# Kernel optimization log

Hardware: AMD Instinct MI355X
Metric: run time of the kernel (lower is better)

Reference implementation:

```python
import jax, jax.numpy as jnp
import numpy as np

THR = 1.0   # snntorch Leaky default threshold
BETA = 0.9  # leak factor from the module


@jax.custom_vjp
def atan_spike(x):
    # Heaviside forward; ATan surrogate gradient (snntorch default alpha=2):
    # d/dx = 1 / (1 + (pi * x)^2)
    return (x > 0).astype(x.dtype)

def _atan_fwd(x):
    return (x > 0).astype(x.dtype), x

def _atan_bwd(x, g):
    return (g / (1.0 + (jnp.pi * x) ** 2),)

atan_spike.defvjp(_atan_fwd, _atan_bwd)


def setup_inputs() -> dict:
    key = jax.random.key(0)
    k0, k1, k2, k3, k4 = jax.random.split(key, 5)
    B, T, L = 256, 1000, 30  # 24 = L - 7 + 1 matches fc1 in_features 16*24
    out_c = 35
    x = jax.random.normal(k0, (B, T, L), dtype=jnp.float32)
    conv_w = jax.random.normal(k1, (16, 1, 7), dtype=jnp.float32) / np.float32(np.sqrt(7.0))
    conv_b = jax.random.normal(k2, (16,), dtype=jnp.float32) * 0.05
    fc_w = jax.random.normal(k3, (out_c, 16 * 24), dtype=jnp.float32) / np.float32(np.sqrt(384.0))
    fc_b = jax.random.normal(k4, (out_c,), dtype=jnp.float32) * 0.05
    return {"x": x, "conv_w": conv_w, "conv_b": conv_b, "fc_w": fc_w, "fc_b": fc_b}


def reference(x, conv_w, conv_b, fc_w, fc_b):
    B, T, L = x.shape
    # Conv1d has no recurrence -> hoist it out of the time loop, batched over B*T.
    cur1 = jax.lax.conv_general_dilated(
        x.reshape(B * T, 1, L), conv_w, window_strides=(1,), padding="VALID",
        dimension_numbers=("NCH", "OIH", "NCH"),
    ) + conv_b[None, :, None]                      # (B*T, 16, 24)
    Lo = cur1.shape[-1]
    cur1 = cur1.reshape(B, T, 16, Lo).transpose(1, 0, 2, 3)  # (T, B, 16, 24)
    out_c = fc_w.shape[0]

    def step(carry, c1):
        mem1, mem2 = carry
        # LIF1: reset-by-subtraction using detached spike of previous membrane
        r1 = jax.lax.stop_gradient((mem1 > THR).astype(mem1.dtype))
        mem1 = BETA * mem1 + c1 - r1 * THR
        spk1 = atan_spike(mem1 - THR)              # (B, 16, 24)
        c2 = spk1.reshape(B, 16 * Lo) @ fc_w.T + fc_b  # (B, out_c)
        # LIF2
        r2 = jax.lax.stop_gradient((mem2 > THR).astype(mem2.dtype))
        mem2 = BETA * mem2 + c2 - r2 * THR
        return (mem1, mem2), mem2

    init = (jnp.zeros((B, 16, Lo), x.dtype), jnp.zeros((B, out_c), x.dtype))
    _, mem2_rec = jax.lax.scan(step, init, cur1)   # (T, B, out_c)
    return mem2_rec.mean(axis=0)                   # (B, out_c)
```

## Files before the change

kernel.cpp:

```cpp
#include <hip/hip_runtime.h>

typedef _Float16 half8 __attribute__((ext_vector_type(8)));
typedef float f32x4 __attribute__((ext_vector_type(4)));

#define SPH  32
#define NIT  34
#define SPKW 392
#define XTW  36
#define C2W  48
#define TN   1000

__global__ __launch_bounds__(768, 1) void snn_fwd(
    const float* __restrict__ x,
    const float* __restrict__ conv_w,
    const float* __restrict__ conv_b,
    const float* __restrict__ fc_w,
    const float* __restrict__ fc_b,
    float* __restrict__ out)
{
    __shared__ __align__(16) _Float16 spk[2][SPH][SPKW];
    __shared__ __align__(16) float    xsT[2][30][XTW];
    __shared__ __align__(16) float    c2L[2][SPH][C2W];

    const int tid  = threadIdx.x;
    const int b    = blockIdx.x;
    const int wid  = tid >> 6;
    const int lane = tid & 63;

    const int ct = tid;
    const int c  = ct / 24;
    const int p  = ct % 24;
    float wk[7];
    float cb = 0.f;
    if (wid < 6) {
#pragma unroll
        for (int k = 0; k < 7; ++k) wk[k] = conv_w[c * 7 + k];
        cb = conv_b[c];
    }

    const int g  = wid - 6;
    const int m  = g >> 1;
    const int tb = g & 1;
    const int nL = lane & 15;
    const int q  = lane >> 4;
    half8 A[12];
    if (wid >= 6) {
        const int o = m * 16 + nL;
#pragma unroll
        for (int kt = 0; kt < 12; ++kt) {
            half8 a;
#pragma unroll
            for (int j = 0; j < 8; ++j) {
                int K = kt * 32 + q * 8 + j;
                a[j] = (o < 35) ? (_Float16)fc_w[o * 384 + K] : (_Float16)0.f;
            }
            A[kt] = a;
        }
    }
    const float fcb = (wid == 6 && lane < 35) ? fc_b[lane] : 0.f;
    const int st = tid - 384;

    float m1 = 0.f, sp = 0.f;
    float mem2 = 0.f, accO = 0.f;

    const float* xb = x + (size_t)b * (TN * 30);

    if (wid >= 6) {
#pragma unroll
        for (int r = 0; r < 3; ++r) {
            int f = st + 384 * r;
            if (f < 960) xsT[0][f % 30][f / 30] = xb[f];
        }
    }
    __syncthreads();

#pragma unroll 1
    for (int ph = 0; ph < NIT; ++ph) {
        if (wid < 6) {
            if (ph < 32) {
                const float* xcol = &xsT[ph & 1][p][0];
                unsigned short* sdst = (unsigned short*)&spk[ph & 1][0][ct];
#pragma unroll 2
                for (int s0 = 0; s0 < SPH; s0 += 4) {
                    f32x4 xv[7];
#pragma unroll
                    for (int k = 0; k < 7; ++k)
                        xv[k] = *(const f32x4*)(xcol + k * XTW + s0);
                    float cc[4];
#pragma unroll
                    for (int dt = 0; dt < 4; ++dt) cc[dt] = cb;
#pragma unroll
                    for (int k = 0; k < 7; ++k) {
#pragma unroll
                        for (int dt = 0; dt < 4; ++dt)
                            cc[dt] = fmaf(wk[k], xv[k][dt], cc[dt]);
                    }
#pragma unroll
                    for (int dt = 0; dt < 4; ++dt) {
                        m1 = fmaf(0.9f, m1, cc[dt] - sp);
                        sp = (m1 > 1.0f) ? 1.0f : 0.0f;
                        sdst[(s0 + dt) * SPKW] =
                            (m1 > 1.0f) ? (unsigned short)0x3C00u : (unsigned short)0u;
                    }
                }
            }
        } else {
            float xr[3];
            const bool stg = (ph <= 30);
            if (stg) {
                const float* src = xb + (ph + 1) * (SPH * 30);
#pragma unroll
                for (int r = 0; r < 3; ++r) {
                    int f = st + 384 * r;
                    int t = (ph + 1) * SPH + f / 30;
                    xr[r] = (f < 960 && t < TN) ? src[f] : 0.f;
                }
            }
            const bool doScan = (wid == 6 && lane < 35 && ph >= 2);
            float v[SPH];
            if (doScan) {
                const float* cs = &c2L[(ph - 2) & 1][0][0];
#pragma unroll
                for (int j = 0; j < SPH; ++j) v[j] = cs[j * C2W + lane];
            }
            if (ph >= 1 && ph <= 32) {
                const _Float16* sb = &spk[(ph - 1) & 1][0][0];
                half8 B[12];
#pragma unroll
                for (int kt = 0; kt < 12; ++kt)
                    B[kt] = *(const half8*)(sb + (tb * 16 + nL) * SPKW + kt * 32 + q * 8);
                f32x4 acc = {0.f, 0.f, 0.f, 0.f};
#pragma unroll
                for (int kt = 0; kt < 12; ++kt)
                    acc = __builtin_amdgcn_mfma_f32_16x16x32_f16(A[kt], B[kt], acc, 0, 0, 0);
                float* cd = &c2L[(ph - 1) & 1][0][0];
                *(f32x4*)(cd + (tb * 16 + nL) * C2W + m * 16 + q * 4) = acc;
            }
            if (doScan) {
                const int tbase = (ph - 2) * SPH;
#pragma unroll
                for (int j = 0; j < SPH; ++j) {
                    float r2 = (mem2 > 1.0f) ? 1.0f : 0.0f;
                    mem2 = 0.9f * mem2 + (v[j] + fcb) - r2;
                    if (tbase + j < TN) accO += mem2;
                }
            }
            if (stg) {
                float* dst = &xsT[(ph + 1) & 1][0][0];
#pragma unroll
                for (int r = 0; r < 3; ++r) {
                    int f = st + 384 * r;
                    if (f < 960) dst[(f % 30) * XTW + (f / 30)] = xr[r];
                }
            }
        }
        __syncthreads();
    }

    if (wid == 6 && lane < 35) out[b * 35 + lane] = accO * (1.0f / (float)TN);
}

extern "C" void kernel_launch(void* const* d_in, const int* in_sizes, int n_in,
                              void* d_out, int out_size, void* d_ws, size_t ws_size,
                              hipStream_t stream) {
    const float* x      = (const float*)d_in[0];
    const float* conv_w = (const float*)d_in[1];
    const float* conv_b = (const float*)d_in[2];
    const float* fc_w   = (const float*)d_in[3];
    const float* fc_b   = (const float*)d_in[4];
    float* out          = (float*)d_out;

    snn_fwd<<<256, 768, 0, stream>>>(x, conv_w, conv_b, fc_w, fc_b, out);
}
```

Measured before the change: 149.9 us.

## Add dedicated staging/scan wavefronts and prefetch input two phases ahead

Grows the block from 12 to 16 wavefronts, so MFMA waves do only the fc matmul and four new waves handle x staging and the LIF2 scan. The global load for x is issued one phase earlier and held in registers across the barrier, which hides global memory latency. The transpose indices are precomputed once. The cost is more threads per block and a changed launch bound, which could affect register allocation.

After: 147.0 us. 1.02x faster.

```diff
diff --git a/kernel.cpp b/kernel.cpp
--- a/kernel.cpp
+++ b/kernel.cpp
@@ -10,7 +10,7 @@
 #define C2W  48
 #define TN   1000
 
-__global__ __launch_bounds__(768, 1) void snn_fwd(
+__global__ __launch_bounds__(1024, 4) void snn_fwd(
     const float* __restrict__ x,
     const float* __restrict__ conv_w,
     const float* __restrict__ conv_b,
@@ -44,7 +44,7 @@
     const int nL = lane & 15;
     const int q  = lane >> 4;
     half8 A[12];
-    if (wid >= 6) {
+    if (wid >= 6 && wid < 12) {
         const int o = m * 16 + nL;
 #pragma unroll
         for (int kt = 0; kt < 12; ++kt) {
@@ -57,19 +57,35 @@
             A[kt] = a;
         }
     }
-    const float fcb = (wid == 6 && lane < 35) ? fc_b[lane] : 0.f;
-    const int st = tid - 384;
+
+    const int st4 = tid - 768;
+    int fs[4], fl[4];
+    if (wid >= 12) {
+#pragma unroll
+        for (int r = 0; r < 4; ++r) {
+            int f = st4 + 256 * r;
+            fs[r] = f / 30;
+            fl[r] = f % 30;
+        }
+    }
+    const float fcb = (wid == 12 && lane < 35) ? fc_b[lane] : 0.f;
 
     float m1 = 0.f, sp = 0.f;
     float mem2 = 0.f, accO = 0.f;
+    float xr[4];
 
     const float* xb = x + (size_t)b * (TN * 30);
 
-    if (wid >= 6) {
+    if (wid >= 12) {
 #pragma unroll
-        for (int r = 0; r < 3; ++r) {
-            int f = st + 384 * r;
-            if (f < 960) xsT[0][f % 30][f / 30] = xb[f];
+        for (int r = 0; r < 4; ++r) {
+            int f = st4 + 256 * r;
+            if (f < 960) xsT[0][fl[r]][fs[r]] = xb[f];
+        }
+#pragma unroll
+        for (int r = 0; r < 4; ++r) {
+            int f = st4 + 256 * r;
+            xr[r] = (f < 960) ? xb[960 + f] : 0.f;
         }
     }
     __syncthreads();
@@ -104,25 +120,7 @@
                     }
                 }
             }
-        } else {
-            float xr[3];
-            const bool stg = (ph <= 30);
-            if (stg) {
-                const float* src = xb + (ph + 1) * (SPH * 30);
-#pragma unroll
-                for (int r = 0; r < 3; ++r) {
-                    int f = st + 384 * r;
-                    int t = (ph + 1) * SPH + f / 30;
-                    xr[r] = (f < 960 && t < TN) ? src[f] : 0.f;
-                }
-            }
-            const bool doScan = (wid == 6 && lane < 35 && ph >= 2);
-            float v[SPH];
-            if (doScan) {
-                const float* cs = &c2L[(ph - 2) & 1][0][0];
-#pragma unroll
-                for (int j = 0; j < SPH; ++j) v[j] = cs[j * C2W + lane];
-            }
+        } else if (wid < 12) {
             if (ph >= 1 && ph <= 32) {
                 const _Float16* sb = &spk[(ph - 1) & 1][0][0];
                 half8 B[12];
@@ -136,7 +134,29 @@
                 float* cd = &c2L[(ph - 1) & 1][0][0];
                 *(f32x4*)(cd + (tb * 16 + nL) * C2W + m * 16 + q * 4) = acc;
             }
-            if (doScan) {
+        } else {
+            if (ph <= 30) {
+                float* dst = &xsT[(ph + 1) & 1][0][0];
+#pragma unroll
+                for (int r = 0; r < 4; ++r) {
+                    int f = st4 + 256 * r;
+                    if (f < 960) dst[fl[r] * XTW + fs[r]] = xr[r];
+                }
+            }
+            if (ph <= 29) {
+                const float* src = xb + (size_t)(ph + 2) * (SPH * 30);
+#pragma unroll
+                for (int r = 0; r < 4; ++r) {
+                    int f = st4 + 256 * r;
+                    int t = (ph + 2) * SPH + fs[r];
+                    xr[r] = (f < 960 && t < TN) ? src[f] : 0.f;
+                }
+            }
+            if (wid == 12 && lane < 35 && ph >= 2) {
+                const float* cs = &c2L[(ph - 2) & 1][0][0];
+                float v[SPH];
+#pragma unroll
+                for (int j = 0; j < SPH; ++j) v[j] = cs[j * C2W + lane];
                 const int tbase = (ph - 2) * SPH;
 #pragma unroll
                 for (int j = 0; j < SPH; ++j) {
@@ -145,19 +165,11 @@
                     if (tbase + j < TN) accO += mem2;
                 }
             }
-            if (stg) {
-                float* dst = &xsT[(ph + 1) & 1][0][0];
-#pragma unroll
-                for (int r = 0; r < 3; ++r) {
-                    int f = st + 384 * r;
-                    if (f < 960) dst[(f % 30) * XTW + (f / 30)] = xr[r];
-                }
-            }
         }
         __syncthreads();
     }
 
-    if (wid == 6 && lane < 35) out[b * 35 + lane] = accO * (1.0f / (float)TN);
+    if (wid == 12 && lane < 35) out[b * 35 + lane] = accO * (1.0f / (float)TN);
 }
 
 extern "C" void kernel_launch(void* const* d_in, const int* in_sizes, int n_in,
@@ -170,5 +182,5 @@
     const float* fc_b   = (const float*)d_in[4];
     float* out          = (float*)d_out;
 
-    snn_fwd<<<256, 768, 0, stream>>>(x, conv_w, conv_b, fc_w, fc_b, out);
+    snn_fwd<<<256, 1024, 0, stream>>>(x, conv_w, conv_b, fc_w, fc_b, out);
 }
```

## Load conv inputs directly from global with register prefetch, drop LDS staging

Applied to the files above, without the earlier changes.

The conv threads now read their 7-tap input windows straight from global memory with unaligned vector loads, prefetching the next four timesteps into registers instead of having MFMA waves stage a transposed x tile in LDS. The conv thread mapping becomes channel-fastest (c = tid&15), and the fc weight matrix is permuted at load time to match the new spike layout. Launch bounds are raised to allow multiple blocks per CU. This removes the LDS staging and transpose traffic but puts redundant, partly overlapping global/L1 loads on the serial LIF recurrence path, and tighter launch bounds may constrain register use.

Result: slower. 206.1 us (+37.4%).

```diff
diff --git a/kernel.cpp b/kernel.cpp
--- a/kernel.cpp
+++ b/kernel.cpp
@@ -2,15 +2,15 @@
 
 typedef _Float16 half8 __attribute__((ext_vector_type(8)));
 typedef float f32x4 __attribute__((ext_vector_type(4)));
+typedef float f32x4u __attribute__((ext_vector_type(4), aligned(4)));
 
 #define SPH  32
 #define NIT  34
 #define SPKW 392
-#define XTW  36
 #define C2W  48
 #define TN   1000
 
-__global__ __launch_bounds__(768, 1) void snn_fwd(
+__global__ __launch_bounds__(768, 3) void snn_fwd(
     const float* __restrict__ x,
     const float* __restrict__ conv_w,
     const float* __restrict__ conv_b,
@@ -19,7 +19,6 @@
     float* __restrict__ out)
 {
     __shared__ __align__(16) _Float16 spk[2][SPH][SPKW];
-    __shared__ __align__(16) float    xsT[2][30][XTW];
     __shared__ __align__(16) float    c2L[2][SPH][C2W];
 
     const int tid  = threadIdx.x;
@@ -28,8 +27,8 @@
     const int lane = tid & 63;
 
     const int ct = tid;
-    const int c  = ct / 24;
-    const int p  = ct % 24;
+    const int c  = ct & 15;
+    const int p  = ct >> 4;
     float wk[7];
     float cb = 0.f;
     if (wid < 6) {
@@ -51,53 +50,62 @@
             half8 a;
 #pragma unroll
             for (int j = 0; j < 8; ++j) {
-                int K = kt * 32 + q * 8 + j;
-                a[j] = (o < 35) ? (_Float16)fc_w[o * 384 + K] : (_Float16)0.f;
+                int Kp = kt * 32 + q * 8 + j;
+                int Kc = Kp & 15;
+                int Kq = Kp >> 4;
+                a[j] = (o < 35) ? (_Float16)fc_w[o * 384 + Kc * 24 + Kq]
+                                : (_Float16)0.f;
             }
             A[kt] = a;
         }
     }
     const float fcb = (wid == 6 && lane < 35) ? fc_b[lane] : 0.f;
-    const int st = tid - 384;
 
     float m1 = 0.f, sp = 0.f;
     float mem2 = 0.f, accO = 0.f;
 
     const float* xb = x + (size_t)b * (TN * 30);
 
-    if (wid >= 6) {
+    f32x4 pA[4], pB[4];
+    if (wid < 6) {
 #pragma unroll
-        for (int r = 0; r < 3; ++r) {
-            int f = st + 384 * r;
-            if (f < 960) xsT[0][f % 30][f / 30] = xb[f];
+        for (int dt = 0; dt < 4; ++dt) {
+            const float* r = xb + dt * 30 + p;
+            pA[dt] = (f32x4)(*(const f32x4u*)r);
+            pB[dt] = (f32x4)(*(const f32x4u*)(r + 3));
         }
     }
-    __syncthreads();
 
 #pragma unroll 1
     for (int ph = 0; ph < NIT; ++ph) {
         if (wid < 6) {
             if (ph < 32) {
-                const float* xcol = &xsT[ph & 1][p][0];
                 unsigned short* sdst = (unsigned short*)&spk[ph & 1][0][ct];
-#pragma unroll 2
+                const int T0 = ph * SPH;
+#pragma unroll
                 for (int s0 = 0; s0 < SPH; s0 += 4) {
-                    f32x4 xv[7];
+                    f32x4 cA[4], cB[4];
 #pragma unroll
-                    for (int k = 0; k < 7; ++k)
-                        xv[k] = *(const f32x4*)(xcol + k * XTW + s0);
-                    float cc[4];
+                    for (int dt = 0; dt < 4; ++dt) { cA[dt] = pA[dt]; cB[dt] = pB[dt]; }
 #pragma unroll
-                    for (int dt = 0; dt < 4; ++dt) cc[dt] = cb;
-#pragma unroll
-                    for (int k = 0; k < 7; ++k) {
-#pragma unroll
-                        for (int dt = 0; dt < 4; ++dt)
-                            cc[dt] = fmaf(wk[k], xv[k][dt], cc[dt]);
+                    for (int dt = 0; dt < 4; ++dt) {
+                        int t = T0 + s0 + 4 + dt;
+                        t = (t < TN) ? t : (TN - 1);
+                        const float* r = xb + t * 30 + p;
+                        pA[dt] = (f32x4)(*(const f32x4u*)r);
+                        pB[dt] = (f32x4)(*(const f32x4u*)(r + 3));
                     }
 #pragma unroll
                     for (int dt = 0; dt < 4; ++dt) {
-                        m1 = fmaf(0.9f, m1, cc[dt] - sp);
+                        float c1 = cb;
+                        c1 = fmaf(wk[0], cA[dt][0], c1);
+                        c1 = fmaf(wk[1], cA[dt][1], c1);
+                        c1 = fmaf(wk[2], cA[dt][2], c1);
+                        c1 = fmaf(wk[3], cA[dt][3], c1);
+                        c1 = fmaf(wk[4], cB[dt][1], c1);
+                        c1 = fmaf(wk[5], cB[dt][2], c1);
+                        c1 = fmaf(wk[6], cB[dt][3], c1);
+                        m1 = fmaf(0.9f, m1, c1 - sp);
                         sp = (m1 > 1.0f) ? 1.0f : 0.0f;
                         sdst[(s0 + dt) * SPKW] =
                             (m1 > 1.0f) ? (unsigned short)0x3C00u : (unsigned short)0u;
@@ -105,24 +113,6 @@
                 }
             }
         } else {
-            float xr[3];
-            const bool stg = (ph <= 30);
-            if (stg) {
-                const float* src = xb + (ph + 1) * (SPH * 30);
-#pragma unroll
-                for (int r = 0; r < 3; ++r) {
-                    int f = st + 384 * r;
-                    int t = (ph + 1) * SPH + f / 30;
-                    xr[r] = (f < 960 && t < TN) ? src[f] : 0.f;
-                }
-            }
-            const bool doScan = (wid == 6 && lane < 35 && ph >= 2);
-            float v[SPH];
-            if (doScan) {
-                const float* cs = &c2L[(ph - 2) & 1][0][0];
-#pragma unroll
-                for (int j = 0; j < SPH; ++j) v[j] = cs[j * C2W + lane];
-            }
             if (ph >= 1 && ph <= 32) {
                 const _Float16* sb = &spk[(ph - 1) & 1][0][0];
                 half8 B[12];
@@ -136,21 +126,17 @@
                 float* cd = &c2L[(ph - 1) & 1][0][0];
                 *(f32x4*)(cd + (tb * 16 + nL) * C2W + m * 16 + q * 4) = acc;
             }
-            if (doScan) {
+            if (wid == 6 && lane < 35 && ph >= 2) {
+                const float* cs = &c2L[(ph - 2) & 1][0][0];
+                float v[SPH];
+#pragma unroll
+                for (int j = 0; j < SPH; ++j) v[j] = cs[j * C2W + lane];
                 const int tbase = (ph - 2) * SPH;
 #pragma unroll
                 for (int j = 0; j < SPH; ++j) {
                     float r2 = (mem2 > 1.0f) ? 1.0f : 0.0f;
                     mem2 = 0.9f * mem2 + (v[j] + fcb) - r2;
                     if (tbase + j < TN) accO += mem2;
-                }
-            }
-            if (stg) {
-                float* dst = &xsT[(ph + 1) & 1][0][0];
-#pragma unroll
-                for (int r = 0; r < 3; ++r) {
-                    int f = st + 384 * r;
-                    if (f < 960) dst[(f % 30) * XTW + (f / 30)] = xr[r];
                 }
             }
         }
```
